# Performance work log

Measured on AMD Instinct MI355X. Metric: run time of the kernel, lower is better.

The kernel has to match this reference:

```python
import jax, jax.numpy as jnp
import numpy as np
import math

B, L, D = 4, 2048, 512
H = 8
HD = D // H
K1 = 64  # local_window_size
K2 = 64  # global_window_size


def semi_local_mask(seq_len):
    # Faithful to create_semi_local_mask: anti-diagonal band + global prefix, ANDed with causal tril.
    i = jnp.arange(seq_len)[:, None]
    j = jnp.arange(seq_len)[None, :]
    band = (i + j >= seq_len - K1) & (i + j <= seq_len)
    glob = (j <= K2) & (j <= seq_len - i)
    causal = j <= i
    return (band | glob) & causal  # [L, L] bool


def setup_inputs() -> dict:
    key = jax.random.key(0)
    ks = jax.random.split(key, 8)
    def xavier(k, shape):
        fan_in, fan_out = shape[1], shape[0]
        lim = math.sqrt(6.0 / (fan_in + fan_out))
        return jax.random.uniform(k, shape, jnp.float32, -lim, lim)
    x = jax.random.normal(ks[0], (B, L, D), jnp.float32)
    w_qkv = xavier(ks[1], (3 * D, D)); b_qkv = jnp.zeros((3 * D,), jnp.float32)
    w_u = xavier(ks[2], (D, D));       b_u = jnp.zeros((D,), jnp.float32)
    w_out = xavier(ks[3], (D, D));     b_out = jnp.zeros((D,), jnp.float32)
    return {"x": x, "w_qkv": w_qkv, "b_qkv": b_qkv, "w_u": w_u, "b_u": b_u,
            "w_out": w_out, "b_out": b_out}


def reference(x, w_qkv, b_qkv, w_u, b_u, w_out, b_out):
    Bsz, Lq, Dm = x.shape
    qkv = (x @ w_qkv.T + b_qkv).reshape(Bsz, Lq, 3, H, HD)
    q, k, v = jnp.moveaxis(qkv, 2, 0)            # each [B, L, H, HD]
    q = jnp.transpose(q, (0, 2, 1, 3))           # [B, H, L, HD]
    k = jnp.transpose(k, (0, 2, 1, 3))
    v = jnp.transpose(v, (0, 2, 1, 3))
    u = x @ w_u.T + b_u                          # [B, L, D] (gate values)
    scale = 1.0 / math.sqrt(HD)
    scores = jnp.einsum('bhqd,bhkd->bhqk', q * scale, k)
    mask = semi_local_mask(Lq)                   # [L, L]
    scores = jnp.where(mask[None, None], scores, -jnp.inf)
    attn = jax.nn.softmax(scores, axis=-1)
    out = jnp.einsum('bhqk,bhkd->bhqd', attn, v)
    out = jnp.transpose(out, (0, 2, 1, 3)).reshape(Bsz, Lq, Dm)
    out = jax.nn.silu(out) * u
    return out @ w_out.T + b_out
```

## Files before the change

### kernel.cpp

```cpp
#include <hip/hip_runtime.h>
#include <hip/hip_bf16.h>

typedef __bf16 bf16x8 __attribute__((ext_vector_type(8)));
typedef float f32x4 __attribute__((ext_vector_type(4)));

#define B_ 4
#define L_ 2048
#define D_ 512
#define H_ 8

__device__ __forceinline__ void gl16(const __bf16* g, __bf16* l) {
  __builtin_amdgcn_global_load_lds(
      (const __attribute__((address_space(1))) void*)g,
      (__attribute__((address_space(3))) void*)l, 16, 0, 0);
}

__global__ __launch_bounds__(256) void cvt_pack(
    const float* __restrict__ x, const float* __restrict__ wq,
    const float* __restrict__ wu, const float* __restrict__ wo,
    const float* __restrict__ bq, const float* __restrict__ bu,
    __bf16* __restrict__ xb, __bf16* __restrict__ wcat,
    __bf16* __restrict__ wob, float* __restrict__ bcat)
{
  const int idx8 = blockIdx.x * 256 + threadIdx.x;
  const float* src; __bf16* dst; size_t so, dof;
  if (idx8 < 524288)      { src = x;  dst = xb;   so = (size_t)idx8 * 8;            dof = so; }
  else if (idx8 < 622592) { src = wq; dst = wcat; so = (size_t)(idx8 - 524288) * 8; dof = so; }
  else if (idx8 < 655360) { src = wu; dst = wcat; so = (size_t)(idx8 - 622592) * 8; dof = so + 786432; }
  else                    { src = wo; dst = wob;  so = (size_t)(idx8 - 655360) * 8; dof = so; }
  const float4 lo = *(const float4*)(src + so);
  const float4 hi = *(const float4*)(src + so + 4);
  bf16x8 r;
  r[0] = (__bf16)lo.x; r[1] = (__bf16)lo.y; r[2] = (__bf16)lo.z; r[3] = (__bf16)lo.w;
  r[4] = (__bf16)hi.x; r[5] = (__bf16)hi.y; r[6] = (__bf16)hi.z; r[7] = (__bf16)hi.w;
  *(bf16x8*)(dst + dof) = r;
  if (blockIdx.x == 0) {
#pragma unroll
    for (int e = 0; e < 8; ++e) {
      const int col = threadIdx.x * 8 + e;
      bcat[col] = (col < 1536) ? bq[col] : bu[col - 1536];
    }
  }
}

template <typename TOUT>
__global__ __launch_bounds__(256) void gemm_async(
    const __bf16* __restrict__ A, const __bf16* __restrict__ W,
    const float* __restrict__ bias, TOUT* __restrict__ C,
    int M, int N, int K)
{
  __shared__ __bf16 lA[4096];
  __shared__ __bf16 lB[4096];
  const int t = threadIdx.x;
  const int lane = t & 63;
  const int wave = t >> 6;
  const int bm0 = blockIdx.x * 128;
  const int bn0 = blockIdx.y * 128;
  const int wm = (wave >> 1) * 64;
  const int wn = (wave & 1) * 64;

  f32x4 acc[4][4] = {};

  const __bf16* Ap0 = A + (size_t)(bm0 + (t >> 2)) * K + (t & 3) * 8;
  const __bf16* Bp0 = W + (size_t)(bn0 + (t >> 2)) * K + (t & 3) * 8;
  const size_t r64 = (size_t)64 * K;

  for (int k0 = 0; k0 < K; k0 += 32) {
    __syncthreads();
    gl16(Ap0 + k0,       lA + t * 8);
    gl16(Ap0 + r64 + k0, lA + (t + 256) * 8);
    gl16(Bp0 + k0,       lB + t * 8);
    gl16(Bp0 + r64 + k0, lB + (t + 256) * 8);
    __syncthreads();

    const int r = lane & 15, q = lane >> 4;
    bf16x8 af[4], bfr[4];
#pragma unroll
    for (int mi = 0; mi < 4; ++mi) af[mi] = ((const bf16x8*)lA)[(wm + mi * 16 + r) * 4 + q];
#pragma unroll
    for (int ni = 0; ni < 4; ++ni) bfr[ni] = ((const bf16x8*)lB)[(wn + ni * 16 + r) * 4 + q];
#pragma unroll
    for (int mi = 0; mi < 4; ++mi)
#pragma unroll
      for (int ni = 0; ni < 4; ++ni)
        acc[mi][ni] = __builtin_amdgcn_mfma_f32_16x16x32_bf16(af[mi], bfr[ni], acc[mi][ni], 0, 0, 0);
  }

  const int cc = lane & 15, cq = lane >> 4;
#pragma unroll
  for (int mi = 0; mi < 4; ++mi) {
#pragma unroll
    for (int ni = 0; ni < 4; ++ni) {
      const int gcol = bn0 + wn + ni * 16 + cc;
      const float bv = bias[gcol];
#pragma unroll
      for (int rr = 0; rr < 4; ++rr) {
        const int grow = bm0 + wm + mi * 16 + cq * 4 + rr;
        C[(size_t)grow * N + gcol] = (TOUT)(acc[mi][ni][rr] + bv);
      }
    }
  }
}

#define SS 69
#define SP 72
#define QS 2048
__global__ __launch_bounds__(256) void attn_tile(
    const __bf16* __restrict__ qu,
    __bf16* __restrict__ g)
{
  const int qt = blockIdx.x, h = blockIdx.y, b = blockIdx.z;
  const int t = threadIdx.x;
  const int lane = t & 63;
  const int w = t >> 6;
  const int q0 = qt * 64, qmax = q0 + 63;
  const size_t bL = (size_t)b * L_;

  __shared__ __bf16 lQ[4096];
  __shared__ __bf16 lK[4096];
  __shared__ __bf16 lV[64 * SP];
  __shared__ float  Ssh[64 * SS];
  __shared__ __bf16 Pb[64 * SP];
  __shared__ float  pmax[256], psum[256];
  __shared__ float  ms[64], lsum[64], corrs[64];

  {
    const int row = t >> 2, gb = t & 3;
    const __bf16* src = qu + (bL + q0 + row) * QS + h * 64;
    ((bf16x8*)lQ)[row * 8 + gb]     = *(const bf16x8*)(src + gb * 8);
    ((bf16x8*)lQ)[row * 8 + gb + 4] = *(const bf16x8*)(src + (gb + 4) * 8);
  }
  if (t < 64) { ms[t] = -1e30f; lsum[t] = 0.f; }

  int clist[5]; int ncl = 0;
  clist[ncl++] = 0;
  if (qmax >= 64) clist[ncl++] = 64;
  {
    int lo = 1921 - q0; if (lo < 0) lo = 0; lo &= ~63;
    const int hik = min(qmax, 2048 - q0);
    for (int c = lo; c <= hik; c += 64)
      if (c >= 128) clist[ncl++] = c;
  }

  f32x4 acc_o[4] = {};
  const int cq = lane >> 4, cc = lane & 15;

  for (int ci = 0; ci < ncl; ++ci) {
    const int c0 = clist[ci];
    __syncthreads();
    {
      const int row = t >> 2, gb = t & 3;
      const __bf16* src = qu + (bL + c0 + row) * QS + 512 + h * 64;
      ((bf16x8*)lK)[row * 8 + gb]     = *(const bf16x8*)(src + gb * 8);
      ((bf16x8*)lK)[row * 8 + gb + 4] = *(const bf16x8*)(src + (gb + 4) * 8);
    }
    {
      const int key = lane;
      const __bf16* src = qu + (bL + c0 + key) * QS + 1024 + h * 64 + w * 16;
      bf16x8 va = *(const bf16x8*)src;
      bf16x8 vb = *(const bf16x8*)(src + 8);
#pragma unroll
      for (int e = 0; e < 8; ++e) {
        lV[(w * 16 + e) * SP + key]     = va[e];
        lV[(w * 16 + 8 + e) * SP + key] = vb[e];
      }
    }
    __syncthreads();

    {
      const int r = cc, q = cq;
#pragma unroll
      for (int nt = 0; nt < 4; ++nt) {
        f32x4 s = {};
        bf16x8 aq0 = *(const bf16x8*)(lQ + (w * 16 + r) * 64 + q * 8);
        bf16x8 aq1 = *(const bf16x8*)(lQ + (w * 16 + r) * 64 + 32 + q * 8);
        bf16x8 bk0 = *(const bf16x8*)(lK + (nt * 16 + r) * 64 + q * 8);
        bf16x8 bk1 = *(const bf16x8*)(lK + (nt * 16 + r) * 64 + 32 + q * 8);
        s = __builtin_amdgcn_mfma_f32_16x16x32_bf16(aq0, bk0, s, 0, 0, 0);
        s = __builtin_amdgcn_mfma_f32_16x16x32_bf16(aq1, bk1, s, 0, 0, 0);
#pragma unroll
        for (int rr = 0; rr < 4; ++rr) {
          const int i = q0 + w * 16 + cq * 4 + rr;
          const int j = c0 + nt * 16 + cc;
          const int ij = i + j;
          const bool valid = (j <= i) &&
              ((ij >= 1984 && ij <= 2048) || (j <= 64 && ij <= 2048));
          Ssh[(w * 16 + cq * 4 + rr) * SS + nt * 16 + cc] =
              valid ? s[rr] * 0.125f : -1e30f;
        }
      }
    }
    __syncthreads();

    {
      float pm = -1e30f;
#pragma unroll
      for (int c = 0; c < 16; ++c) pm = fmaxf(pm, Ssh[lane * SS + w * 16 + c]);
      pmax[w * 64 + lane] = pm;
    }
    __syncthreads();
    if (t < 64) {
      float nm = ms[t];
#pragma unroll
      for (int q4 = 0; q4 < 4; ++q4) nm = fmaxf(nm, pmax[q4 * 64 + t]);
      corrs[t] = __expf(ms[t] - nm);
      ms[t] = nm;
    }
    __syncthreads();
    {
      const float nm = ms[lane];
      float ps = 0.f;
      bf16x8 p8a, p8b;
#pragma unroll
      for (int c = 0; c < 8; ++c) {
        const float p = __expf(Ssh[lane * SS + w * 16 + c] - nm);
        p8a[c] = (__bf16)p; ps += p;
      }
#pragma unroll
      for (int c = 0; c < 8; ++c) {
        const float p = __expf(Ssh[lane * SS + w * 16 + 8 + c] - nm);
        p8b[c] = (__bf16)p; ps += p;
      }
      *(bf16x8*)(Pb + lane * SP + w * 16)     = p8a;
      *(bf16x8*)(Pb + lane * SP + w * 16 + 8) = p8b;
      psum[w * 64 + lane] = ps;
    }
    __syncthreads();
    if (t < 64)
      lsum[t] = lsum[t] * corrs[t] + psum[t] + psum[64 + t] + psum[128 + t] + psum[192 + t];

    {
      const int r = cc, q = cq;
      float cr[4];
#pragma unroll
      for (int rr = 0; rr < 4; ++rr) cr[rr] = corrs[w * 16 + cq * 4 + rr];
#pragma unroll
      for (int dt = 0; dt < 4; ++dt) {
#pragma unroll
        for (int rr = 0; rr < 4; ++rr) acc_o[dt][rr] *= cr[rr];
        bf16x8 pa0 = *(const bf16x8*)(Pb + (w * 16 + r) * SP + q * 8);
        bf16x8 pa1 = *(const bf16x8*)(Pb + (w * 16 + r) * SP + 32 + q * 8);
        bf16x8 vb0 = *(const bf16x8*)(lV + (dt * 16 + r) * SP + q * 8);
        bf16x8 vb1 = *(const bf16x8*)(lV + (dt * 16 + r) * SP + 32 + q * 8);
        acc_o[dt] = __builtin_amdgcn_mfma_f32_16x16x32_bf16(pa0, vb0, acc_o[dt], 0, 0, 0);
        acc_o[dt] = __builtin_amdgcn_mfma_f32_16x16x32_bf16(pa1, vb1, acc_o[dt], 0, 0, 0);
      }
    }
  }
  __syncthreads();

#pragma unroll
  for (int dt = 0; dt < 4; ++dt) {
#pragma unroll
    for (int rr = 0; rr < 4; ++rr) {
      const int row16 = cq * 4 + rr;
      const size_t qrow = bL + q0 + w * 16 + row16;
      const int d = dt * 16 + cc;
      const float o = acc_o[dt][rr] / fmaxf(lsum[w * 16 + row16], 1e-30f);
      const float uv = (float)qu[qrow * QS + 1536 + h * 64 + d];
      g[qrow * D_ + h * 64 + d] = (__bf16)(o / (1.f + __expf(-o)) * uv);
    }
  }
}

extern "C" void kernel_launch(void* const* d_in, const int* in_sizes, int n_in,
                              void* d_out, int out_size, void* d_ws, size_t ws_size,
                              hipStream_t stream) {
  const float* x     = (const float*)d_in[0];
  const float* w_qkv = (const float*)d_in[1];
  const float* b_qkv = (const float*)d_in[2];
  const float* w_u   = (const float*)d_in[3];
  const float* b_u   = (const float*)d_in[4];
  const float* w_out = (const float*)d_in[5];
  const float* b_out = (const float*)d_in[6];
  float* out = (float*)d_out;

  char* ws = (char*)d_ws;
  __bf16* xb   = (__bf16*)ws;
  __bf16* wcat = (__bf16*)(ws + 8388608);
  __bf16* wob  = (__bf16*)(ws + 10485760);
  float*  bcat = (float*) (ws + 11010048);
  __bf16* qu   = (__bf16*)(ws + 11018240);
  __bf16* gb   = (__bf16*)(ws + 44572672);

  cvt_pack<<<dim3(2688), dim3(256), 0, stream>>>(
      x, w_qkv, w_u, w_out, b_qkv, b_u, xb, wcat, wob, bcat);
  gemm_async<__bf16><<<dim3(64, 16), dim3(256), 0, stream>>>(
      xb, wcat, bcat, qu, 8192, 2048, 512);
  attn_tile<<<dim3(L_ / 64, H_, B_), dim3(256), 0, stream>>>(qu, gb);
  gemm_async<float><<<dim3(64, 4), dim3(256), 0, stream>>>(
      gb, wob, b_out, out, 8192, 512, 512);
}
```

Baseline: 164.6 us.

## Keep online softmax in registers with wave shuffles and swizzle K in LDS

```diff
diff --git a/kernel.cpp b/kernel.cpp
--- a/kernel.cpp
+++ b/kernel.cpp
@@ -102,7 +102,6 @@
   }
 }
 
-#define SS 69
 #define SP 72
 #define QS 2048
 __global__ __launch_bounds__(256) void attn_tile(
@@ -116,21 +115,23 @@
   const int q0 = qt * 64, qmax = q0 + 63;
   const size_t bL = (size_t)b * L_;
 
-  __shared__ __bf16 lQ[4096];
   __shared__ __bf16 lK[4096];
   __shared__ __bf16 lV[64 * SP];
-  __shared__ float  Ssh[64 * SS];
   __shared__ __bf16 Pb[64 * SP];
-  __shared__ float  pmax[256], psum[256];
-  __shared__ float  ms[64], lsum[64], corrs[64];
-
+
+  const int cq = lane >> 4, cc = lane & 15;
+
+  bf16x8 aq0, aq1;
   {
-    const int row = t >> 2, gb = t & 3;
-    const __bf16* src = qu + (bL + q0 + row) * QS + h * 64;
-    ((bf16x8*)lQ)[row * 8 + gb]     = *(const bf16x8*)(src + gb * 8);
-    ((bf16x8*)lQ)[row * 8 + gb + 4] = *(const bf16x8*)(src + (gb + 4) * 8);
-  }
-  if (t < 64) { ms[t] = -1e30f; lsum[t] = 0.f; }
+    const __bf16* qsrc = qu + (bL + q0 + w * 16 + cc) * QS + h * 64 + cq * 8;
+    aq0 = *(const bf16x8*)qsrc;
+    aq1 = *(const bf16x8*)(qsrc + 32);
+  }
+
+  float mreg[4], lreg[4];
+#pragma unroll
+  for (int rr = 0; rr < 4; ++rr) { mreg[rr] = -1e30f; lreg[rr] = 0.f; }
+  f32x4 acc_o[4] = {};
 
   int clist[5]; int ncl = 0;
   clist[ncl++] = 0;
@@ -142,17 +143,18 @@
       if (c >= 128) clist[ncl++] = c;
   }
 
-  f32x4 acc_o[4] = {};
-  const int cq = lane >> 4, cc = lane & 15;
-
   for (int ci = 0; ci < ncl; ++ci) {
     const int c0 = clist[ci];
     __syncthreads();
     {
       const int row = t >> 2, gb = t & 3;
       const __bf16* src = qu + (bL + c0 + row) * QS + 512 + h * 64;
-      ((bf16x8*)lK)[row * 8 + gb]     = *(const bf16x8*)(src + gb * 8);
-      ((bf16x8*)lK)[row * 8 + gb + 4] = *(const bf16x8*)(src + (gb + 4) * 8);
+      bf16x8 k0 = *(const bf16x8*)(src + gb * 8);
+      bf16x8 k1 = *(const bf16x8*)(src + gb * 8 + 32);
+      char* lkb = (char*)lK;
+      const int sw = (row & 7) << 4;
+      *(bf16x8*)(lkb + ((row * 128 + gb * 16) ^ sw))      = k0;
+      *(bf16x8*)(lkb + ((row * 128 + gb * 16 + 64) ^ sw)) = k1;
     }
     {
       const int key = lane;
@@ -167,87 +169,86 @@
     }
     __syncthreads();
 
-    {
-      const int r = cc, q = cq;
+    f32x4 s[4];
+    {
+      const char* lkb = (const char*)lK;
 #pragma unroll
       for (int nt = 0; nt < 4; ++nt) {
-        f32x4 s = {};
-        bf16x8 aq0 = *(const bf16x8*)(lQ + (w * 16 + r) * 64 + q * 8);
-        bf16x8 aq1 = *(const bf16x8*)(lQ + (w * 16 + r) * 64 + 32 + q * 8);
-        bf16x8 bk0 = *(const bf16x8*)(lK + (nt * 16 + r) * 64 + q * 8);
-        bf16x8 bk1 = *(const bf16x8*)(lK + (nt * 16 + r) * 64 + 32 + q * 8);
-        s = __builtin_amdgcn_mfma_f32_16x16x32_bf16(aq0, bk0, s, 0, 0, 0);
-        s = __builtin_amdgcn_mfma_f32_16x16x32_bf16(aq1, bk1, s, 0, 0, 0);
-#pragma unroll
-        for (int rr = 0; rr < 4; ++rr) {
-          const int i = q0 + w * 16 + cq * 4 + rr;
-          const int j = c0 + nt * 16 + cc;
-          const int ij = i + j;
-          const bool valid = (j <= i) &&
-              ((ij >= 1984 && ij <= 2048) || (j <= 64 && ij <= 2048));
-          Ssh[(w * 16 + cq * 4 + rr) * SS + nt * 16 + cc] =
-              valid ? s[rr] * 0.125f : -1e30f;
-        }
-      }
-    }
-    __syncthreads();
-
-    {
-      float pm = -1e30f;
-#pragma unroll
-      for (int c = 0; c < 16; ++c) pm = fmaxf(pm, Ssh[lane * SS + w * 16 + c]);
-      pmax[w * 64 + lane] = pm;
-    }
-    __syncthreads();
-    if (t < 64) {
-      float nm = ms[t];
-#pragma unroll
-      for (int q4 = 0; q4 < 4; ++q4) nm = fmaxf(nm, pmax[q4 * 64 + t]);
-      corrs[t] = __expf(ms[t] - nm);
-      ms[t] = nm;
-    }
-    __syncthreads();
-    {
-      const float nm = ms[lane];
-      float ps = 0.f;
-      bf16x8 p8a, p8b;
-#pragma unroll
-      for (int c = 0; c < 8; ++c) {
-        const float p = __expf(Ssh[lane * SS + w * 16 + c] - nm);
-        p8a[c] = (__bf16)p; ps += p;
-      }
-#pragma unroll
-      for (int c = 0; c < 8; ++c) {
-        const float p = __expf(Ssh[lane * SS + w * 16 + 8 + c] - nm);
-        p8b[c] = (__bf16)p; ps += p;
-      }
-      *(bf16x8*)(Pb + lane * SP + w * 16)     = p8a;
-      *(bf16x8*)(Pb + lane * SP + w * 16 + 8) = p8b;
-      psum[w * 64 + lane] = ps;
-    }
-    __syncthreads();
-    if (t < 64)
-      lsum[t] = lsum[t] * corrs[t] + psum[t] + psum[64 + t] + psum[128 + t] + psum[192 + t];
-
-    {
-      const int r = cc, q = cq;
-      float cr[4];
-#pragma unroll
-      for (int rr = 0; rr < 4; ++rr) cr[rr] = corrs[w * 16 + cq * 4 + rr];
+        const int krow = nt * 16 + cc;
+        const int sw = (krow & 7) << 4;
+        bf16x8 bk0 = *(const bf16x8*)(lkb + ((krow * 128 + cq * 16) ^ sw));
+        bf16x8 bk1 = *(const bf16x8*)(lkb + ((krow * 128 + 64 + cq * 16) ^ sw));
+        f32x4 a = {};
+        a = __builtin_amdgcn_mfma_f32_16x16x32_bf16(aq0, bk0, a, 0, 0, 0);
+        a = __builtin_amdgcn_mfma_f32_16x16x32_bf16(aq1, bk1, a, 0, 0, 0);
+        s[nt] = a;
+      }
+    }
+
+#pragma unroll
+    for (int nt = 0; nt < 4; ++nt) {
+#pragma unroll
+      for (int rr = 0; rr < 4; ++rr) {
+        const int i = q0 + w * 16 + cq * 4 + rr;
+        const int j = c0 + nt * 16 + cc;
+        const int ij = i + j;
+        const bool valid = (j <= i) &&
+            ((ij >= 1984 && ij <= 2048) || (j <= 64 && ij <= 2048));
+        s[nt][rr] = valid ? s[nt][rr] * 0.125f : -1e30f;
+      }
+    }
+
+    f32x4 pm;
+#pragma unroll
+    for (int rr = 0; rr < 4; ++rr)
+      pm[rr] = fmaxf(fmaxf(s[0][rr], s[1][rr]), fmaxf(s[2][rr], s[3][rr]));
+#pragma unroll
+    for (int m = 1; m < 16; m <<= 1) {
+#pragma unroll
+      for (int rr = 0; rr < 4; ++rr)
+        pm[rr] = fmaxf(pm[rr], __shfl_xor(pm[rr], m, 64));
+    }
+    float corr[4];
+#pragma unroll
+    for (int rr = 0; rr < 4; ++rr) {
+      const float nm = fmaxf(mreg[rr], pm[rr]);
+      corr[rr] = __expf(mreg[rr] - nm);
+      mreg[rr] = nm;
+    }
+
+    f32x4 ps = {};
+#pragma unroll
+    for (int nt = 0; nt < 4; ++nt) {
+#pragma unroll
+      for (int rr = 0; rr < 4; ++rr) {
+        const float p = __expf(s[nt][rr] - mreg[rr]);
+        ps[rr] += p;
+        Pb[(w * 16 + cq * 4 + rr) * SP + nt * 16 + cc] = (__bf16)p;
+      }
+    }
+#pragma unroll
+    for (int m = 1; m < 16; m <<= 1) {
+#pragma unroll
+      for (int rr = 0; rr < 4; ++rr)
+        ps[rr] += __shfl_xor(ps[rr], m, 64);
+    }
+#pragma unroll
+    for (int rr = 0; rr < 4; ++rr) lreg[rr] = lreg[rr] * corr[rr] + ps[rr];
+
+    {
+      bf16x8 pa0 = *(const bf16x8*)(Pb + (w * 16 + cc) * SP + cq * 8);
+      bf16x8 pa1 = *(const bf16x8*)(Pb + (w * 16 + cc) * SP + 32 + cq * 8);
 #pragma unroll
       for (int dt = 0; dt < 4; ++dt) {
 #pragma unroll
-        for (int rr = 0; rr < 4; ++rr) acc_o[dt][rr] *= cr[rr];
-        bf16x8 pa0 = *(const bf16x8*)(Pb + (w * 16 + r) * SP + q * 8);
-        bf16x8 pa1 = *(const bf16x8*)(Pb + (w * 16 + r) * SP + 32 + q * 8);
-        bf16x8 vb0 = *(const bf16x8*)(lV + (dt * 16 + r) * SP + q * 8);
-        bf16x8 vb1 = *(const bf16x8*)(lV + (dt * 16 + r) * SP + 32 + q * 8);
+        for (int rr = 0; rr < 4; ++rr) acc_o[dt][rr] *= corr[rr];
+        bf16x8 vb0 = *(const bf16x8*)(lV + (dt * 16 + cc) * SP + cq * 8);
+        bf16x8 vb1 = *(const bf16x8*)(lV + (dt * 16 + cc) * SP + 32 + cq * 8);
         acc_o[dt] = __builtin_amdgcn_mfma_f32_16x16x32_bf16(pa0, vb0, acc_o[dt], 0, 0, 0);
         acc_o[dt] = __builtin_amdgcn_mfma_f32_16x16x32_bf16(pa1, vb1, acc_o[dt], 0, 0, 0);
       }
     }
   }
-  __syncthreads();
 
 #pragma unroll
   for (int dt = 0; dt < 4; ++dt) {
@@ -256,7 +257,7 @@
       const int row16 = cq * 4 + rr;
       const size_t qrow = bL + q0 + w * 16 + row16;
       const int d = dt * 16 + cc;
-      const float o = acc_o[dt][rr] / fmaxf(lsum[w * 16 + row16], 1e-30f);
+      const float o = acc_o[dt][rr] / fmaxf(lreg[rr], 1e-30f);
       const float uv = (float)qu[qrow * QS + 1536 + h * 64 + d];
       g[qrow * D_ + h * 64 + d] = (__bf16)(o / (1.f + __expf(-o)) * uv);
     }
```

After: 158.2 us. 3.9% less time.
